# Optimization experiments

Measured on AMD Instinct MI355X. Metric: run time of the kernel, lower is better.

## Reference

```python
import jax, jax.numpy as jnp
import numpy as np

FIXED_FRAMES = 30
# MediaPipe Holistic landmark layout: 468 face, 21 left hand, 33 pose, 21 right hand = 543
LIPS = np.array([61, 185, 40, 39, 37, 0, 267, 269, 270, 409, 291,
                 146, 91, 181, 84, 17, 314, 405, 321, 375,
                 78, 191, 80, 81, 82, 13, 312, 311, 310, 415,
                 95, 88, 178, 87, 14, 317, 402, 318, 324, 308], dtype=np.int32)
LEFT_HAND = np.arange(468, 489, dtype=np.int32)          # 21
UPPER_BODY = np.arange(489, 489 + 25, dtype=np.int32)    # 25 upper-body pose landmarks
RIGHT_HAND = np.arange(522, 543, dtype=np.int32)         # 21
SEL = np.concatenate([LIPS, LEFT_HAND, UPPER_BODY, RIGHT_HAND])  # 107 landmarks

N_FRAMES = 16384
N_LANDMARKS = 543

def setup_inputs() -> dict:
    key = jax.random.key(0)
    k1, k2 = jax.random.split(key)
    x = jax.random.normal(k1, (N_FRAMES, N_LANDMARKS, 3), dtype=jnp.float32)
    nan_mask = jax.random.uniform(k2, x.shape) < 0.1
    x = jnp.where(nan_mask, jnp.nan, x)
    return {"x_in": x}

def _normalize_gather(x_in):
    # Global nan-aware mean over ALL elements (scalar), as x[~isnan(x)].mean()
    mask = ~jnp.isnan(x_in)
    cnt = jnp.sum(mask).astype(x_in.dtype)
    xs = jnp.where(mask, x_in, 0.0)
    mean = jnp.sum(xs) / cnt
    xc = jnp.where(mask, x_in - mean, 0.0)
    # torch.std of the centered non-NaN values (unbiased, re-subtracts its own mean)
    m2 = jnp.sum(xc) / cnt
    var = jnp.sum(jnp.where(mask, (xc - m2) ** 2, 0.0)) / (cnt - 1.0)
    std = jnp.sqrt(var)
    y = jnp.where(mask, xc / std, 0.0)  # normalize; NaN positions -> 0 (x[isnan]=0)
    return y[:, SEL, :]                  # gather lips|lhand|pose|rhand -> [T, 107, 3]

def _resample(y, T):
    # F.interpolate over frame axis to FIXED_FRAMES (static Python branch on shape)
    if T < FIXED_FRAMES:
        # mode='linear', align_corners=False
        pos = (jnp.arange(FIXED_FRAMES, dtype=y.dtype) + 0.5) * (T / FIXED_FRAMES) - 0.5
        pos = jnp.clip(pos, 0.0, T - 1.0)
        i0 = jnp.floor(pos).astype(jnp.int32)
        i1 = jnp.minimum(i0 + 1, T - 1)
        w = (pos - i0.astype(y.dtype))[:, None, None]
        return (1.0 - w) * y[i0] + w * y[i1]
    else:
        # mode='nearest-exact'
        idx = jnp.floor((jnp.arange(FIXED_FRAMES, dtype=jnp.float32) + 0.5) * (T / FIXED_FRAMES))
        idx = jnp.clip(idx.astype(jnp.int32), 0, T - 1)
        return y[idx]

def reference(x_in):
    T = x_in.shape[0]
    y = _normalize_gather(x_in)   # [T, 107, 3]
    return _resample(y, T)        # [30, 107, 3]
```

## Files before the change

### kernel.cpp

```cpp
#include <hip/hip_runtime.h>

#define FIXED_FRAMES 30
#define N_LM 543
#define N_SEL 107
#define NBLK 2048
#define NTHR 256

__constant__ int c_sel[N_SEL] = {
    61, 185, 40, 39, 37, 0, 267, 269, 270, 409, 291,
    146, 91, 181, 84, 17, 314, 405, 321, 375,
    78, 191, 80, 81, 82, 13, 312, 311, 310, 415,
    95, 88, 178, 87, 14, 317, 402, 318, 324, 308,
    468, 469, 470, 471, 472, 473, 474, 475, 476, 477, 478,
    479, 480, 481, 482, 483, 484, 485, 486, 487, 488,
    489, 490, 491, 492, 493, 494, 495, 496, 497, 498, 499,
    500, 501, 502, 503, 504, 505, 506, 507, 508, 509, 510,
    511, 512, 513,
    522, 523, 524, 525, 526, 527, 528, 529, 530, 531, 532,
    533, 534, 535, 536, 537, 538, 539, 540, 541, 542
};


__device__ __forceinline__ void acc4(float4 v, double& s, double& s2, unsigned& c) {
    float vals[4] = {v.x, v.y, v.z, v.w};
#pragma unroll
    for (int k = 0; k < 4; ++k) {
        float f = vals[k];
        bool ok = (f == f);
        float fz = ok ? f : 0.0f;
        double d = (double)fz;
        s += d;
        s2 += d * d;
        c += ok ? 1u : 0u;
    }
}

__global__ __launch_bounds__(NTHR) void fp_reduce(const float4* __restrict__ x, int n4,
                                                  double* __restrict__ ws) {
    double s = 0.0, s2 = 0.0;
    unsigned int c = 0;

    int idx = blockIdx.x * NTHR + threadIdx.x;
    const int stride = NBLK * NTHR;

    int i = idx;
    for (; i + stride < n4; i += 2 * stride) {
        float4 v0 = x[i];
        float4 v1 = x[i + stride];
        acc4(v0, s, s2, c);
        acc4(v1, s, s2, c);
    }
    if (i < n4) acc4(x[i], s, s2, c);

#pragma unroll
    for (int off = 32; off > 0; off >>= 1) {
        s  += __shfl_down(s, off, 64);
        s2 += __shfl_down(s2, off, 64);
        c  += __shfl_down(c, off, 64);
    }

    __shared__ double ls[4], ls2[4];
    __shared__ unsigned int lc[4];
    int lane = threadIdx.x & 63;
    int wave = threadIdx.x >> 6;
    if (lane == 0) { ls[wave] = s; ls2[wave] = s2; lc[wave] = c; }
    __syncthreads();
    if (threadIdx.x == 0) {
        double bs = 0.0, bs2 = 0.0;
        unsigned long long bc = 0;
#pragma unroll
        for (int w = 0; w < 4; ++w) { bs += ls[w]; bs2 += ls2[w]; bc += lc[w]; }
        ws[blockIdx.x]            = bs;
        ws[NBLK + blockIdx.x]     = bs2;
        ws[2 * NBLK + blockIdx.x] = (double)bc;
    }
}

__global__ __launch_bounds__(NTHR) void fp_final(double* __restrict__ ws) {
    double s = 0.0, s2 = 0.0, c = 0.0;
    for (int i = threadIdx.x; i < NBLK; i += NTHR) {
        s  += ws[i];
        s2 += ws[NBLK + i];
        c  += ws[2 * NBLK + i];
    }
#pragma unroll
    for (int off = 32; off > 0; off >>= 1) {
        s  += __shfl_down(s, off, 64);
        s2 += __shfl_down(s2, off, 64);
        c  += __shfl_down(c, off, 64);
    }
    __shared__ double ls[4], ls2[4], lc[4];
    int lane = threadIdx.x & 63;
    int wave = threadIdx.x >> 6;
    if (lane == 0) { ls[wave] = s; ls2[wave] = s2; lc[wave] = c; }
    __syncthreads();
    if (threadIdx.x == 0) {
        double S1 = 0.0, S2 = 0.0, dc = 0.0;
#pragma unroll
        for (int w = 0; w < 4; ++w) { S1 += ls[w]; S2 += ls2[w]; dc += lc[w]; }

        double mean = S1 / dc;
        double m2 = (S1 - dc * mean) / dc;
        double mu = mean + m2;
        double var = (S2 - 2.0 * mu * S1 + dc * mu * mu) / (dc - 1.0);
        double inv_std = 1.0 / sqrt(var);

        ws[3 * NBLK]     = mean;
        ws[3 * NBLK + 1] = inv_std;
    }
}

__global__ void fp_gather(const float* __restrict__ x, const double* __restrict__ ws,
                          float* __restrict__ out, int T) {
    int t = blockIdx.x * blockDim.x + threadIdx.x;
    const int total = FIXED_FRAMES * N_SEL * 3;
    if (t >= total) return;

    double mean = ws[3 * NBLK];
    double inv_std = ws[3 * NBLK + 1];

    int f = t / (N_SEL * 3);
    int r = t - f * (N_SEL * 3);
    int l = r / 3;
    int ch = r - l * 3;

    float scale = (float)T / 30.0f;
    int fi = (int)floorf(((float)f + 0.5f) * scale);
    if (fi > T - 1) fi = T - 1;
    if (fi < 0) fi = 0;

    float v = x[(size_t)fi * (N_LM * 3) + (size_t)c_sel[l] * 3 + ch];
    out[t] = (v == v) ? (float)(((double)v - mean) * inv_std) : 0.0f;
}

extern "C" void kernel_launch(void* const* d_in, const int* in_sizes, int n_in,
                              void* d_out, int out_size, void* d_ws, size_t ws_size,
                              hipStream_t stream) {
    const float* x = (const float*)d_in[0];
    float* out = (float*)d_out;
    double* ws = (double*)d_ws;

    int n = in_sizes[0];
    int n4 = n / 4;
    int T = n / (N_LM * 3);

    fp_reduce<<<NBLK, NTHR, 0, stream>>>((const float4*)x, n4, ws);
    fp_final<<<1, NTHR, 0, stream>>>(ws);

    const int total = FIXED_FRAMES * N_SEL * 3;
    fp_gather<<<(total + 255) / 256, 256, 0, stream>>>(x, ws, out, T);
}
```

Measured before the change: 29.41 us.

## Use fp32 per-thread accumulation, unroll loads 4x, fuse final reduce into gather

Per-thread sums and sums of squares now accumulate in float with fmaf and are widened to double only for the cross-lane and cross-block reduction. This avoids slow FP64 adds in the hot loop. The main loop now issues four float4 loads per iteration instead of two. The separate final-reduction kernel is removed, and every gather block recomputes the global statistics from the per-block partials, saving one launch at the cost of redundant reads of those partials. Float accumulation over about 13 elements per thread may lose a little precision.

```diff
diff --git a/kernel.cpp b/kernel.cpp
--- a/kernel.cpp
+++ b/kernel.cpp
@@ -21,49 +21,53 @@
 };
 
 
-__device__ __forceinline__ void acc4(float4 v, double& s, double& s2, unsigned& c) {
+__device__ __forceinline__ void acc4f(float4 v, float& s, float& s2, unsigned& c) {
     float vals[4] = {v.x, v.y, v.z, v.w};
 #pragma unroll
     for (int k = 0; k < 4; ++k) {
         float f = vals[k];
         bool ok = (f == f);
         float fz = ok ? f : 0.0f;
-        double d = (double)fz;
-        s += d;
-        s2 += d * d;
-        c += ok ? 1u : 0u;
+        s  += fz;
+        s2 = fmaf(fz, fz, s2);
+        c  += ok ? 1u : 0u;
     }
 }
 
 __global__ __launch_bounds__(NTHR) void fp_reduce(const float4* __restrict__ x, int n4,
                                                   double* __restrict__ ws) {
-    double s = 0.0, s2 = 0.0;
+    float s = 0.0f, s2 = 0.0f;
     unsigned int c = 0;
 
     int idx = blockIdx.x * NTHR + threadIdx.x;
     const int stride = NBLK * NTHR;
 
     int i = idx;
-    for (; i + stride < n4; i += 2 * stride) {
+    for (; i + 3 * stride < n4; i += 4 * stride) {
         float4 v0 = x[i];
         float4 v1 = x[i + stride];
-        acc4(v0, s, s2, c);
-        acc4(v1, s, s2, c);
+        float4 v2 = x[i + 2 * stride];
+        float4 v3 = x[i + 3 * stride];
+        acc4f(v0, s, s2, c);
+        acc4f(v1, s, s2, c);
+        acc4f(v2, s, s2, c);
+        acc4f(v3, s, s2, c);
     }
-    if (i < n4) acc4(x[i], s, s2, c);
+    for (; i < n4; i += stride) acc4f(x[i], s, s2, c);
 
+    double sd = (double)s, s2d = (double)s2;
 #pragma unroll
     for (int off = 32; off > 0; off >>= 1) {
-        s  += __shfl_down(s, off, 64);
-        s2 += __shfl_down(s2, off, 64);
-        c  += __shfl_down(c, off, 64);
+        sd  += __shfl_down(sd, off, 64);
+        s2d += __shfl_down(s2d, off, 64);
+        c   += __shfl_down(c, off, 64);
     }
 
     __shared__ double ls[4], ls2[4];
     __shared__ unsigned int lc[4];
     int lane = threadIdx.x & 63;
     int wave = threadIdx.x >> 6;
-    if (lane == 0) { ls[wave] = s; ls2[wave] = s2; lc[wave] = c; }
+    if (lane == 0) { ls[wave] = sd; ls2[wave] = s2d; lc[wave] = c; }
     __syncthreads();
     if (threadIdx.x == 0) {
         double bs = 0.0, bs2 = 0.0;
@@ -76,7 +80,9 @@
     }
 }
 
-__global__ __launch_bounds__(NTHR) void fp_final(double* __restrict__ ws) {
+__global__ __launch_bounds__(NTHR) void fp_gather(const float* __restrict__ x,
+                                                  const double* __restrict__ ws,
+                                                  float* __restrict__ out, int T) {
     double s = 0.0, s2 = 0.0, c = 0.0;
     for (int i = threadIdx.x; i < NBLK; i += NTHR) {
         s  += ws[i];
@@ -90,6 +96,7 @@
         c  += __shfl_down(c, off, 64);
     }
     __shared__ double ls[4], ls2[4], lc[4];
+    __shared__ double sm_mean, sm_inv_std;
     int lane = threadIdx.x & 63;
     int wave = threadIdx.x >> 6;
     if (lane == 0) { ls[wave] = s; ls2[wave] = s2; lc[wave] = c; }
@@ -103,21 +110,17 @@
         double m2 = (S1 - dc * mean) / dc;
         double mu = mean + m2;
         double var = (S2 - 2.0 * mu * S1 + dc * mu * mu) / (dc - 1.0);
-        double inv_std = 1.0 / sqrt(var);
+        sm_mean = mean;
+        sm_inv_std = 1.0 / sqrt(var);
+    }
+    __syncthreads();
 
-        ws[3 * NBLK]     = mean;
-        ws[3 * NBLK + 1] = inv_std;
-    }
-}
-
-__global__ void fp_gather(const float* __restrict__ x, const double* __restrict__ ws,
-                          float* __restrict__ out, int T) {
-    int t = blockIdx.x * blockDim.x + threadIdx.x;
+    int t = blockIdx.x * NTHR + threadIdx.x;
     const int total = FIXED_FRAMES * N_SEL * 3;
     if (t >= total) return;
 
-    double mean = ws[3 * NBLK];
-    double inv_std = ws[3 * NBLK + 1];
+    double mean = sm_mean;
+    double inv_std = sm_inv_std;
 
     int f = t / (N_SEL * 3);
     int r = t - f * (N_SEL * 3);
@@ -145,8 +148,7 @@
     int T = n / (N_LM * 3);
 
     fp_reduce<<<NBLK, NTHR, 0, stream>>>((const float4*)x, n4, ws);
-    fp_final<<<1, NTHR, 0, stream>>>(ws);
 
     const int total = FIXED_FRAMES * N_SEL * 3;
-    fp_gather<<<(total + 255) / 256, 256, 0, stream>>>(x, ws, out, T);
+    fp_gather<<<(total + NTHR - 1) / NTHR, NTHR, 0, stream>>>(x, ws, out, T);
 }
```

Measured after the change: 28.17 us. 1.04x faster.
